# Optimization experiments

Hardware: AMD Instinct MI355X
Metric: run time of the kernel (lower is better)

Reference implementation:

```python
import jax, jax.numpy as jnp
import numpy as np

D_BRICK = 512  # args.brick_vector_dimension
H = 512        # hidden width


def setup_inputs() -> dict:
    key = jax.random.key(0)
    ks = jax.random.split(key, 20)
    B, N = 4, 192

    def w(k, shape, fan_in):
        return jax.random.uniform(k, shape, jnp.float32, -1.0, 1.0) / np.sqrt(fan_in)

    return {
        "brick_vectors": jax.random.normal(ks[0], (B, N, D_BRICK), jnp.float32),
        "xy": jax.random.uniform(ks[1], (B, N, 2), jnp.float32),
        # linear_xy: 2 -> 512
        "W_xy": w(ks[2], (H, 2), 2), "b_xy": w(ks[3], (H,), 2),
        # linear_a: D -> 512
        "W_a": w(ks[4], (H, D_BRICK), D_BRICK), "b_a": w(ks[5], (H,), D_BRICK),
        # linear_b: 512 -> 512
        "W_b": w(ks[6], (H, H), H), "b_b": w(ks[7], (H,), H),
        # combination_a: 1024 -> 512
        "W_ca": w(ks[8], (H, 2 * H), 2 * H), "b_ca": w(ks[9], (H,), 2 * H),
        # combination_b: 512 -> 512
        "W_cb": w(ks[10], (H, H), H), "b_cb": w(ks[11], (H,), H),
        # combination_c: 512 -> 512
        "W_cc": w(ks[12], (H, H), H), "b_cc": w(ks[13], (H,), H),
        # edge_out: 512 -> 2
        "W_out": w(ks[14], (2, H), H), "b_out": w(ks[15], (2,), H),
    }


def reference(brick_vectors, xy, W_xy, b_xy, W_a, b_a, W_b, b_b,
              W_ca, b_ca, W_cb, b_cb, W_cc, b_cc, W_out, b_out):
    # per-brick feature MLP: (B, N, 512)
    f = jnp.einsum('bnd,hd->bnh', brick_vectors, W_a) + b_a \
        + jnp.einsum('bnt,ht->bnh', xy, W_xy) + b_xy
    f = jax.nn.relu(f)
    f = jax.nn.relu(jnp.einsum('bnh,gh->bng', f, W_b) + b_b)

    # combination_a on concat(f[b,j], f[b,i]) without materializing the
    # (B, N, N, 1024) tensor: split the weight into the two 512 halves.
    # edge[b,i,j] = cat(features_a, features_b) where features_a = f[b,j]
    # (expanded over dim 1) and features_b = f[b,i] (expanded over dim 2).
    W1, W2 = W_ca[:, :H], W_ca[:, H:]
    u = jnp.einsum('bnh,gh->bng', f, W1)  # contribution from f[b, j]
    v = jnp.einsum('bnh,gh->bng', f, W2)  # contribution from f[b, i]
    e = jax.nn.relu(u[:, None, :, :] + v[:, :, None, :] + b_ca)  # (B,N,N,512)

    e = jax.nn.relu(jnp.einsum('bijh,gh->bijg', e, W_cb) + b_cb)
    e = jax.nn.relu(jnp.einsum('bijh,gh->bijg', e, W_cc) + b_cc)
    return jnp.einsum('bijh,oh->bijo', e, W_out) + b_out  # (B, N, N, 2)
```

## Files before the change

### kernel.cpp

```cpp
#include <hip/hip_runtime.h>


typedef short  short8  __attribute__((ext_vector_type(8)));
typedef short  short4v __attribute__((ext_vector_type(4)));
typedef float  f32x4   __attribute__((ext_vector_type(4)));

#define LDSW 520

__device__ inline unsigned short f2bf(float x) {
  unsigned u = __float_as_uint(x);
  unsigned r = (u + 0x7FFFu + ((u >> 16) & 1u)) >> 16;
  return (unsigned short)r;
}

__device__ __host__ inline int wtile_off(int c, int k) {
  return ((c >> 4) * 16 + (k >> 5)) * 512 + (c & 15) * 32 + (k & 31);
}

template <int MT, int NT>
__device__ inline void zero_acc(f32x4 (&acc)[MT][NT]) {
#pragma unroll
  for (int mt = 0; mt < MT; ++mt)
#pragma unroll
    for (int nt = 0; nt < NT; ++nt) {
      f32x4 z = {0.f, 0.f, 0.f, 0.f};
      acc[mt][nt] = z;
    }
}

template <int MT, int NT>
__device__ inline void gemm_kloop(const short* E, const short* __restrict__ W,
                                  int lane, int nbase, f32x4 (&acc)[MT][NT]) {
  const int mrow = lane & 15, kg = lane >> 4;
  const short* El = E + mrow * LDSW + kg * 8;
  const short* Wl = W + (nbase >> 4) * 8192 + mrow * 32 + kg * 8;
  short8 wF[2][NT];
#pragma unroll
  for (int nt = 0; nt < NT; ++nt) wF[0][nt] = *(const short8*)(Wl + nt * 8192);
#pragma unroll
  for (int ks = 0; ks < 16; ++ks) {
    const int cur = ks & 1, nxt = cur ^ 1;
    if (ks < 15) {
      const int k1 = (ks + 1) * 512;
#pragma unroll
      for (int nt = 0; nt < NT; ++nt)
        wF[nxt][nt] = *(const short8*)(Wl + nt * 8192 + k1);
    }
    const int k0 = ks * 32;
    short8 e0 = *(const short8*)(El + k0);
#pragma unroll
    for (int mt = 0; mt < MT; ++mt) {
      const short8 ecur = e0;
      if (mt < MT - 1) e0 = *(const short8*)(El + (mt + 1) * 16 * LDSW + k0);
#pragma unroll
      for (int nt = 0; nt < NT; ++nt)
        acc[mt][nt] = __builtin_amdgcn_mfma_f32_16x16x32_bf16(
            wF[cur][nt], ecur, acc[mt][nt], 0, 0, 0);
    }
  }
}

template <int MT, int NT>
__device__ inline void store_relu_lds(short* E, const float* __restrict__ bias,
                                      int lane, int nbase, f32x4 (&acc)[MT][NT]) {
  const int mrow = lane & 15, kg = lane >> 4;
#pragma unroll
  for (int nt = 0; nt < NT; ++nt) {
    const int oc = nbase + nt * 16 + kg * 4;
    const float4 bs = *(const float4*)(bias + oc);
#pragma unroll
    for (int mt = 0; mt < MT; ++mt) {
      short4v s;
      s.x = (short)f2bf(fmaxf(acc[mt][nt][0] + bs.x, 0.f));
      s.y = (short)f2bf(fmaxf(acc[mt][nt][1] + bs.y, 0.f));
      s.z = (short)f2bf(fmaxf(acc[mt][nt][2] + bs.z, 0.f));
      s.w = (short)f2bf(fmaxf(acc[mt][nt][3] + bs.w, 0.f));
      *(short4v*)&E[(mt * 16 + mrow) * LDSW + oc] = s;
    }
  }
}

__global__ void prep_kernel(const float* __restrict__ Wa, const float* __restrict__ Wb,
                            const float* __restrict__ Wca, const float* __restrict__ Wcb,
                            const float* __restrict__ Wcc, const float* __restrict__ Wout,
                            short* __restrict__ outS) {
  const int tid = blockIdx.x * blockDim.x + threadIdx.x;
  const int stride = gridDim.x * blockDim.x;
  const int M = 262144;
  for (int i = tid; i < 6 * M + 1024; i += stride) {
    float x;
    int dst;
    if (i < M) {
      const int c = i >> 9, k = i & 511;
      x = Wa[i];
      dst = wtile_off(c, k);
    } else if (i < 2 * M) {
      const int t = i - M, c = t >> 9, k = t & 511;
      x = Wb[t];
      dst = M + wtile_off(c, k);
    } else if (i < 3 * M) {
      const int t = i - 2 * M, c = t >> 9, k = t & 511;
      x = Wca[c * 1024 + k];
      dst = 2 * M + wtile_off(c, k);
    } else if (i < 4 * M) {
      const int t = i - 3 * M, c = t >> 9, k = t & 511;
      x = Wca[c * 1024 + 512 + k];
      dst = 2 * M + wtile_off(512 + c, k);
    } else if (i < 5 * M) {
      const int t = i - 4 * M, c = t >> 9, k = t & 511;
      x = Wcb[t];
      dst = 4 * M + wtile_off(c, k);
    } else if (i < 6 * M) {
      const int t = i - 5 * M, c = t >> 9, k = t & 511;
      x = Wcc[t];
      dst = 5 * M + wtile_off(c, k);
    } else {
      x = Wout[i - 6 * M];
      dst = i;
    }
    outS[dst] = (short)f2bf(x);
  }
}

template <int MODE>
__global__ __launch_bounds__(256, 4) void node_layer(
    const void* __restrict__ Xin, const short* __restrict__ W,
    const float* __restrict__ bias, const float* __restrict__ xy,
    const float* __restrict__ Wxy, const float* __restrict__ bxy,
    void* __restrict__ Yout, float* __restrict__ vout, int colTiles) {
  __shared__ short X[16 * LDSW];
  __shared__ float xyl[32];
  const int tid = threadIdx.x, lane = tid & 63, wave = tid >> 6;
  const int rt = blockIdx.x / colTiles, ct = blockIdx.x % colTiles;
  const int row0 = rt * 16, c0 = ct * 64;

  if (MODE == 1) {
    const float* bv = (const float*)Xin;
    const int hc = (tid & 127) * 4, m0 = tid >> 7;
    for (int m = m0; m < 16; m += 2) {
      const float4 t = *(const float4*)(bv + (row0 + m) * 512 + hc);
      short4v s;
      s.x = (short)f2bf(t.x); s.y = (short)f2bf(t.y);
      s.z = (short)f2bf(t.z); s.w = (short)f2bf(t.w);
      *(short4v*)&X[m * LDSW + hc] = s;
    }
    if (tid < 32) xyl[tid] = xy[row0 * 2 + tid];
  } else {
    const short* xb = (const short*)Xin;
    const int hc = (tid & 63) * 8, m0 = tid >> 6;
    for (int m = m0; m < 16; m += 4)
      *(short8*)&X[m * LDSW + hc] = *(const short8*)(xb + (row0 + m) * 512 + hc);
  }
  __syncthreads();

  const int nbase = c0 + wave * 16;
  f32x4 acc[1][1];
  zero_acc<1, 1>(acc);
  gemm_kloop<1, 1>(X, W, lane, nbase, acc);

  const int mrow = lane & 15, kg = lane >> 4;
  const int oc = nbase + kg * 4;
  if (MODE == 3) {
    float* u = (float*)Yout;
    const int row = row0 + mrow;
    if (oc < 512) *(f32x4*)&u[row * 512 + oc] = acc[0][0];
    else          *(f32x4*)&vout[row * 512 + oc - 512] = acc[0][0];
  } else {
    short* Y = (short*)Yout;
    const float4 bs = *(const float4*)(bias + oc);
    float b2[4] = {0.f, 0.f, 0.f, 0.f}, w0[4], w1[4];
    if (MODE == 1) {
      const float4 t = *(const float4*)(bxy + oc);
      b2[0] = t.x; b2[1] = t.y; b2[2] = t.z; b2[3] = t.w;
#pragma unroll
      for (int r = 0; r < 4; ++r) { w0[r] = Wxy[(oc + r) * 2]; w1[r] = Wxy[(oc + r) * 2 + 1]; }
    }
    const int row = mrow;
    short4v s;
#pragma unroll
    for (int r = 0; r < 4; ++r) {
      float xv = acc[0][0][r] + ((const float*)&bs)[r];
      if (MODE == 1) xv += b2[r] + xyl[row * 2] * w0[r] + xyl[row * 2 + 1] * w1[r];
      ((short*)&s)[r] = (short)f2bf(fmaxf(xv, 0.f));
    }
    *(short4v*)&Y[(row0 + row) * 512 + oc] = s;
  }
}

__global__ __launch_bounds__(512, 2) void edge_kernel(
    const float* __restrict__ u, const float* __restrict__ v,
    const short* __restrict__ Wcb, const short* __restrict__ Wcc,
    const short* __restrict__ Wout,
    const float* __restrict__ bca, const float* __restrict__ bcb,
    const float* __restrict__ bcc, const float* __restrict__ bout,
    float* __restrict__ out) {
  __shared__ short A[144 * LDSW];
  __shared__ float red[144 * 2 * 8];
  const int tid = threadIdx.x, lane = tid & 63, wave = tid >> 6;
  const int blk = blockIdx.x;
  const int b = blk >> 8, rem = blk & 255, ip = rem >> 2, jt = rem & 3;
  const float* urow0 = u + (b * 192 + jt * 48) * 512;
  const float* vrow0 = v + (b * 192 + ip * 3) * 512;

  {
    const int hc = (tid & 127) * 4, m0 = tid >> 7;
    const float4 v0 = *(const float4*)(vrow0 + hc);
    const float4 v1 = *(const float4*)(vrow0 + 512 + hc);
    const float4 v2 = *(const float4*)(vrow0 + 1024 + hc);
    const float4 bb = *(const float4*)(bca + hc);
#pragma unroll 4
    for (int m = m0; m < 144; m += 4) {
      const int ii = (m >= 96) ? 2 : (m >= 48 ? 1 : 0);
      const int jj = m - ii * 48;
      const float4 vv = (ii == 0) ? v0 : (ii == 1) ? v1 : v2;
      const float4 uu = *(const float4*)(urow0 + jj * 512 + hc);
      short4v s;
      s.x = (short)f2bf(fmaxf(uu.x + vv.x + bb.x, 0.f));
      s.y = (short)f2bf(fmaxf(uu.y + vv.y + bb.y, 0.f));
      s.z = (short)f2bf(fmaxf(uu.z + vv.z + bb.z, 0.f));
      s.w = (short)f2bf(fmaxf(uu.w + vv.w + bb.w, 0.f));
      *(short4v*)&A[m * LDSW + hc] = s;
    }
  }
  __syncthreads();

  const int nbase = wave * 64;
  f32x4 acc[9][4];

  zero_acc<9, 4>(acc);
  gemm_kloop<9, 4>(A, Wcb, lane, nbase, acc);
  __syncthreads();
  store_relu_lds<9, 4>(A, bcb, lane, nbase, acc);
  __syncthreads();

  zero_acc<9, 4>(acc);
  gemm_kloop<9, 4>(A, Wcc, lane, nbase, acc);
  __syncthreads();
  store_relu_lds<9, 4>(A, bcc, lane, nbase, acc);
  __syncthreads();

  f32x4 oacc[9];
#pragma unroll
  for (int mt = 0; mt < 9; ++mt) { f32x4 z = {0.f, 0.f, 0.f, 0.f}; oacc[mt] = z; }
  const int n = lane & 15, kg2 = lane >> 4;
#pragma unroll
  for (int kk = 0; kk < 2; ++kk) {
    const int k0 = wave * 64 + kk * 32 + kg2 * 8;
    short8 bf = {0, 0, 0, 0, 0, 0, 0, 0};
    if (n < 2) bf = *(const short8*)(Wout + n * 512 + k0);
#pragma unroll
    for (int mt = 0; mt < 9; ++mt) {
      const short8 af = *(const short8*)(A + (mt * 16 + n) * LDSW + k0);
      oacc[mt] = __builtin_amdgcn_mfma_f32_16x16x32_bf16(af, bf, oacc[mt], 0, 0, 0);
    }
  }
  if (n < 2) {
#pragma unroll
    for (int mt = 0; mt < 9; ++mt)
#pragma unroll
      for (int r = 0; r < 4; ++r) {
        const int row = mt * 16 + kg2 * 4 + r;
        red[(row * 2 + n) * 8 + wave] = oacc[mt][r];
      }
  }
  __syncthreads();
  if (tid < 288) {
    const int row = tid >> 1, o = tid & 1;
    float s = bout[o];
#pragma unroll
    for (int w = 0; w < 8; ++w) s += red[(row * 2 + o) * 8 + w];
    const int ii = (row >= 96) ? 2 : (row >= 48 ? 1 : 0);
    const int jj = row - ii * 48;
    out[((b * 192 + ip * 3 + ii) * 192 + jt * 48 + jj) * 2 + o] = s;
  }
}

extern "C" void kernel_launch(void* const* d_in, const int* in_sizes, int n_in,
                              void* d_out, int out_size, void* d_ws, size_t ws_size,
                              hipStream_t stream) {
  const float* bv   = (const float*)d_in[0];
  const float* xy   = (const float*)d_in[1];
  const float* Wxy  = (const float*)d_in[2];
  const float* bxy  = (const float*)d_in[3];
  const float* Wa   = (const float*)d_in[4];
  const float* ba   = (const float*)d_in[5];
  const float* Wb   = (const float*)d_in[6];
  const float* bb   = (const float*)d_in[7];
  const float* Wca  = (const float*)d_in[8];
  const float* bca  = (const float*)d_in[9];
  const float* Wcb  = (const float*)d_in[10];
  const float* bcb  = (const float*)d_in[11];
  const float* Wcc  = (const float*)d_in[12];
  const float* bcc  = (const float*)d_in[13];
  const float* Wout = (const float*)d_in[14];
  const float* bout = (const float*)d_in[15];
  float* out = (float*)d_out;

  short* S = (short*)d_ws;
  char* base = (char*)d_ws;
  short* WaB   = S;
  short* WbB   = S + 262144;
  short* WuvB  = S + 524288;
  short* WcbB  = S + 1048576;
  short* WccB  = S + 1310720;
  short* WoutB = S + 1572864;
  short* f1 = (short*)(base + 3147776);
  float* u  = (float*)(base + 3147776);
  short* f2 = (short*)(base + 4720640);
  float* v  = (float*)(base + 5507072);

  prep_kernel<<<512, 256, 0, stream>>>(Wa, Wb, Wca, Wcb, Wcc, Wout, S);
  node_layer<1><<<384, 256, 0, stream>>>(bv, WaB, ba, xy, Wxy, bxy, f1, nullptr, 8);
  node_layer<2><<<384, 256, 0, stream>>>(f1, WbB, bb, nullptr, nullptr, nullptr, f2, nullptr, 8);
  node_layer<3><<<768, 256, 0, stream>>>(f2, WuvB, nullptr, nullptr, nullptr, nullptr, u, v, 16);
  edge_kernel<<<1024, 512, 0, stream>>>(u, v, WcbB, WccB, WoutB, bca, bcb, bcc, bout, out);
}
```

Measured before the change: 248.9 us.

## Switch edge GEMMs to 32x32x16 MFMA with 128-row tiles and retiled weights

```diff
diff --git a/kernel.cpp b/kernel.cpp
--- a/kernel.cpp
+++ b/kernel.cpp
@@ -4,6 +4,7 @@
 typedef short  short8  __attribute__((ext_vector_type(8)));
 typedef short  short4v __attribute__((ext_vector_type(4)));
 typedef float  f32x4   __attribute__((ext_vector_type(4)));
+typedef float  f32x16  __attribute__((ext_vector_type(16)));
 
 #define LDSW 520
 
@@ -16,6 +17,9 @@
 __device__ __host__ inline int wtile_off(int c, int k) {
   return ((c >> 4) * 16 + (k >> 5)) * 512 + (c & 15) * 32 + (k & 31);
 }
+__device__ __host__ inline int wtile_off32(int c, int k) {
+  return ((c >> 5) * 32 + (k >> 4)) * 512 + (c & 31) * 16 + (k & 15);
+}
 
 template <int MT, int NT>
 __device__ inline void zero_acc(f32x4 (&acc)[MT][NT]) {
@@ -24,6 +28,17 @@
 #pragma unroll
     for (int nt = 0; nt < NT; ++nt) {
       f32x4 z = {0.f, 0.f, 0.f, 0.f};
+      acc[mt][nt] = z;
+    }
+}
+
+template <int MT, int NT>
+__device__ inline void zero_acc32(f32x16 (&acc)[MT][NT]) {
+#pragma unroll
+  for (int mt = 0; mt < MT; ++mt)
+#pragma unroll
+    for (int nt = 0; nt < NT; ++nt) {
+      f32x16 z = {};
       acc[mt][nt] = z;
     }
 }
@@ -55,6 +70,38 @@
 #pragma unroll
       for (int nt = 0; nt < NT; ++nt)
         acc[mt][nt] = __builtin_amdgcn_mfma_f32_16x16x32_bf16(
+            wF[cur][nt], ecur, acc[mt][nt], 0, 0, 0);
+    }
+  }
+}
+
+template <int MT, int NT>
+__device__ inline void gemm_kloop32(const short* E, const short* __restrict__ W,
+                                    int lane, int nbase, f32x16 (&acc)[MT][NT]) {
+  const int er = lane & 31, kg = lane >> 5;
+  const short* El = E + er * LDSW + kg * 8;
+  const short* Wl = W + (nbase >> 5) * 16384 + er * 16 + kg * 8;
+  short8 wF[2][NT];
+#pragma unroll
+  for (int nt = 0; nt < NT; ++nt) wF[0][nt] = *(const short8*)(Wl + nt * 16384);
+#pragma unroll
+  for (int ks = 0; ks < 32; ++ks) {
+    const int cur = ks & 1, nxt = cur ^ 1;
+    if (ks < 31) {
+      const int k1 = (ks + 1) * 512;
+#pragma unroll
+      for (int nt = 0; nt < NT; ++nt)
+        wF[nxt][nt] = *(const short8*)(Wl + nt * 16384 + k1);
+    }
+    const int k0 = ks * 16;
+    short8 e0 = *(const short8*)(El + k0);
+#pragma unroll
+    for (int mt = 0; mt < MT; ++mt) {
+      const short8 ecur = e0;
+      if (mt < MT - 1) e0 = *(const short8*)(El + (mt + 1) * 32 * LDSW + k0);
+#pragma unroll
+      for (int nt = 0; nt < NT; ++nt)
+        acc[mt][nt] = __builtin_amdgcn_mfma_f32_32x32x16_bf16(
             wF[cur][nt], ecur, acc[mt][nt], 0, 0, 0);
     }
   }
@@ -76,6 +123,29 @@
       s.z = (short)f2bf(fmaxf(acc[mt][nt][2] + bs.z, 0.f));
       s.w = (short)f2bf(fmaxf(acc[mt][nt][3] + bs.w, 0.f));
       *(short4v*)&E[(mt * 16 + mrow) * LDSW + oc] = s;
+    }
+  }
+}
+
+template <int MT, int NT>
+__device__ inline void store_relu_lds32(short* E, const float* __restrict__ bias,
+                                        int lane, int nbase, f32x16 (&acc)[MT][NT]) {
+  const int er = lane & 31, kh = lane >> 5;
+#pragma unroll
+  for (int nt = 0; nt < NT; ++nt) {
+#pragma unroll
+    for (int rg = 0; rg < 4; ++rg) {
+      const int oc = nbase + nt * 32 + rg * 8 + kh * 4;
+      const float4 bs = *(const float4*)(bias + oc);
+#pragma unroll
+      for (int mt = 0; mt < MT; ++mt) {
+        short4v s;
+        s.x = (short)f2bf(fmaxf(acc[mt][nt][rg * 4 + 0] + bs.x, 0.f));
+        s.y = (short)f2bf(fmaxf(acc[mt][nt][rg * 4 + 1] + bs.y, 0.f));
+        s.z = (short)f2bf(fmaxf(acc[mt][nt][rg * 4 + 2] + bs.z, 0.f));
+        s.w = (short)f2bf(fmaxf(acc[mt][nt][rg * 4 + 3] + bs.w, 0.f));
+        *(short4v*)&E[(mt * 32 + er) * LDSW + oc] = s;
+      }
     }
   }
 }
@@ -109,11 +179,11 @@
     } else if (i < 5 * M) {
       const int t = i - 4 * M, c = t >> 9, k = t & 511;
       x = Wcb[t];
-      dst = 4 * M + wtile_off(c, k);
+      dst = 4 * M + wtile_off32(c, k);
     } else if (i < 6 * M) {
       const int t = i - 5 * M, c = t >> 9, k = t & 511;
       x = Wcc[t];
-      dst = 5 * M + wtile_off(c, k);
+      dst = 5 * M + wtile_off32(c, k);
     } else {
       x = Wout[i - 6 * M];
       dst = i;
@@ -194,26 +264,23 @@
     const float* __restrict__ bca, const float* __restrict__ bcb,
     const float* __restrict__ bcc, const float* __restrict__ bout,
     float* __restrict__ out) {
-  __shared__ short A[144 * LDSW];
-  __shared__ float red[144 * 2 * 8];
+  __shared__ short A[128 * LDSW];
+  __shared__ float red[128 * 2 * 8];
   const int tid = threadIdx.x, lane = tid & 63, wave = tid >> 6;
   const int blk = blockIdx.x;
-  const int b = blk >> 8, rem = blk & 255, ip = rem >> 2, jt = rem & 3;
-  const float* urow0 = u + (b * 192 + jt * 48) * 512;
-  const float* vrow0 = v + (b * 192 + ip * 3) * 512;
+  const int b = blk / 288, rem = blk % 288, ip = rem / 3, jt = rem % 3;
+  const float* urow0 = u + (b * 192 + jt * 64) * 512;
+  const float* vrow0 = v + (b * 192 + ip * 2) * 512;
 
   {
     const int hc = (tid & 127) * 4, m0 = tid >> 7;
     const float4 v0 = *(const float4*)(vrow0 + hc);
     const float4 v1 = *(const float4*)(vrow0 + 512 + hc);
-    const float4 v2 = *(const float4*)(vrow0 + 1024 + hc);
     const float4 bb = *(const float4*)(bca + hc);
 #pragma unroll 4
-    for (int m = m0; m < 144; m += 4) {
-      const int ii = (m >= 96) ? 2 : (m >= 48 ? 1 : 0);
-      const int jj = m - ii * 48;
-      const float4 vv = (ii == 0) ? v0 : (ii == 1) ? v1 : v2;
-      const float4 uu = *(const float4*)(urow0 + jj * 512 + hc);
+    for (int m = m0; m < 128; m += 4) {
+      const float4 vv = (m >= 64) ? v1 : v0;
+      const float4 uu = *(const float4*)(urow0 + (m & 63) * 512 + hc);
       short4v s;
       s.x = (short)f2bf(fmaxf(uu.x + vv.x + bb.x, 0.f));
       s.y = (short)f2bf(fmaxf(uu.y + vv.y + bb.y, 0.f));
@@ -225,23 +292,23 @@
   __syncthreads();
 
   const int nbase = wave * 64;
-  f32x4 acc[9][4];
-
-  zero_acc<9, 4>(acc);
-  gemm_kloop<9, 4>(A, Wcb, lane, nbase, acc);
-  __syncthreads();
-  store_relu_lds<9, 4>(A, bcb, lane, nbase, acc);
-  __syncthreads();
-
-  zero_acc<9, 4>(acc);
-  gemm_kloop<9, 4>(A, Wcc, lane, nbase, acc);
-  __syncthreads();
-  store_relu_lds<9, 4>(A, bcc, lane, nbase, acc);
-  __syncthreads();
-
-  f32x4 oacc[9];
-#pragma unroll
-  for (int mt = 0; mt < 9; ++mt) { f32x4 z = {0.f, 0.f, 0.f, 0.f}; oacc[mt] = z; }
+  f32x16 acc[4][2];
+
+  zero_acc32<4, 2>(acc);
+  gemm_kloop32<4, 2>(A, Wcb, lane, nbase, acc);
+  __syncthreads();
+  store_relu_lds32<4, 2>(A, bcb, lane, nbase, acc);
+  __syncthreads();
+
+  zero_acc32<4, 2>(acc);
+  gemm_kloop32<4, 2>(A, Wcc, lane, nbase, acc);
+  __syncthreads();
+  store_relu_lds32<4, 2>(A, bcc, lane, nbase, acc);
+  __syncthreads();
+
+  f32x4 oacc[8];
+#pragma unroll
+  for (int mt = 0; mt < 8; ++mt) { f32x4 z = {0.f, 0.f, 0.f, 0.f}; oacc[mt] = z; }
   const int n = lane & 15, kg2 = lane >> 4;
 #pragma unroll
   for (int kk = 0; kk < 2; ++kk) {
@@ -249,14 +316,14 @@
     short8 bf = {0, 0, 0, 0, 0, 0, 0, 0};
     if (n < 2) bf = *(const short8*)(Wout + n * 512 + k0);
 #pragma unroll
-    for (int mt = 0; mt < 9; ++mt) {
+    for (int mt = 0; mt < 8; ++mt) {
       const short8 af = *(const short8*)(A + (mt * 16 + n) * LDSW + k0);
       oacc[mt] = __builtin_amdgcn_mfma_f32_16x16x32_bf16(af, bf, oacc[mt], 0, 0, 0);
     }
   }
   if (n < 2) {
 #pragma unroll
-    for (int mt = 0; mt < 9; ++mt)
+    for (int mt = 0; mt < 8; ++mt)
 #pragma unroll
       for (int r = 0; r < 4; ++r) {
         const int row = mt * 16 + kg2 * 4 + r;
@@ -264,14 +331,13 @@
       }
   }
   __syncthreads();
-  if (tid < 288) {
+  if (tid < 256) {
     const int row = tid >> 1, o = tid & 1;
     float s = bout[o];
 #pragma unroll
     for (int w = 0; w < 8; ++w) s += red[(row * 2 + o) * 8 + w];
-    const int ii = (row >= 96) ? 2 : (row >= 48 ? 1 : 0);
-    const int jj = row - ii * 48;
-    out[((b * 192 + ip * 3 + ii) * 192 + jt * 48 + jj) * 2 + o] = s;
+    const int ii = row >> 6, jj = row & 63;
+    out[((b * 192 + ip * 2 + ii) * 192 + jt * 64 + jj) * 2 + o] = s;
   }
 }
 
@@ -313,5 +379,5 @@
   node_layer<1><<<384, 256, 0, stream>>>(bv, WaB, ba, xy, Wxy, bxy, f1, nullptr, 8);
   node_layer<2><<<384, 256, 0, stream>>>(f1, WbB, bb, nullptr, nullptr, nullptr, f2, nullptr, 8);
   node_layer<3><<<768, 256, 0, stream>>>(f2, WuvB, nullptr, nullptr, nullptr, nullptr, u, v, 16);
-  edge_kernel<<<1024, 512, 0, stream>>>(u, v, WcbB, WccB, WoutB, bca, bcb, bcc, bout, out);
-}
+  edge_kernel<<<1152, 512, 0, stream>>>(u, v, WcbB, WccB, WoutB, bca, bcb, bcc, bout, out);
+}
```

Measured after the change: 262.0 us. +5.3%, slower.
